# Optimization experiments

Hardware: AMD Instinct MI355X
Metric: run time of the kernel (lower is better)

## Reference

```python
import jax, jax.numpy as jnp
import numpy as np

B, S, D, H, DH, FF = 4, 4096, 1024, 16, 64, 2048
EPS = 1e-6


def setup_inputs() -> dict:
    key = jax.random.key(0)
    ks = jax.random.split(key, 8)
    s = 0.02
    return {
        "x": jax.random.normal(ks[0], (B, S, D), jnp.float32),
        "scale": jnp.ones((D,), jnp.float32),
        "qw": jax.random.normal(ks[1], (DH * H, D), jnp.float32) * s,
        "qb": jnp.zeros((DH * H,), jnp.float32),
        "kw": jax.random.normal(ks[2], (DH * H, D), jnp.float32) * s,
        "kb": jnp.zeros((DH * H,), jnp.float32),
        "vw": jax.random.normal(ks[3], (DH * H, D), jnp.float32) * s,
        "vb": jnp.zeros((DH * H,), jnp.float32),
        "ow": jax.random.normal(ks[4], (D, DH * H), jnp.float32) * s,
        "ob": jnp.zeros((D,), jnp.float32),
        "f1w": jax.random.normal(ks[5], (FF, D), jnp.float32) * s,
        "f1b": jnp.zeros((FF,), jnp.float32),
        "f2w": jax.random.normal(ks[6], (D, FF), jnp.float32) * s,
        "f2b": jnp.zeros((D,), jnp.float32),
    }


def reference(x, scale, qw, qb, kw, kb, vw, vb, ow, ob, f1w, f1b, f2w, f2b):
    def rms(h):
        return h / jnp.sqrt(jnp.mean(h * h, axis=-1, keepdims=True) + EPS) * scale

    # --- attention (faithful to the module's unusual permutes) ---
    xn = rms(x)
    q = (xn @ qw.T + qb).reshape(B, S, DH, H).transpose(0, 3, 2, 1)  # [B,H,DH,S]
    k = (xn @ kw.T + kb).reshape(B, S, DH, H).transpose(0, 3, 1, 2)  # [B,H,S,DH]
    v = (xn @ vw.T + vb).reshape(B, S, DH, H).transpose(0, 3, 2, 1)  # [B,H,DH,S]
    # scores contract over the SEQUENCE axis -> [B,H,DH,DH]
    att = jax.nn.softmax(jnp.einsum('bhds,bhse->bhde', q, k) / jnp.sqrt(jnp.float32(DH)), axis=-1)
    a = jnp.einsum('bhde,bhes->bhds', att, v)  # [B,H,DH,S]
    # torch: permute(0,2,1,3).reshape(B,-1,DH*H); row-major split of (DH,H,S) -> (S, DH*H)
    a = a.transpose(0, 2, 1, 3).reshape(B, S, DH * H)
    x = a @ ow.T + ob + x

    # --- FFN with the repo's 'SwiGLU' = x*sigmoid(x) + x ---
    xn = rms(x)
    h = xn @ f1w.T + f1b
    h = h * jax.nn.sigmoid(h) + h
    x = h @ f2w.T + f2b + x
    return x
```

## Files before the change

### kernel.cpp

```cpp
#include <hip/hip_runtime.h>
#include <math.h>

typedef unsigned short u16;
typedef __attribute__((ext_vector_type(4))) unsigned short us4;
typedef __attribute__((ext_vector_type(8))) unsigned short us8;
typedef __attribute__((ext_vector_type(4))) float f4;
typedef __attribute__((ext_vector_type(8))) short bf16x8;
typedef __attribute__((ext_vector_type(4))) float f32x4;

#define S_LEN   4096
#define D_MODEL 1024
#define N_HEAD  16
#define D_HEAD  64
#define FF_DIM  2048
#define TOKENS  16384

__device__ __forceinline__ float bf2f(u16 u) {
  union { float f; unsigned u; } x; x.u = ((unsigned)u) << 16; return x.f;
}
__device__ __forceinline__ u16 f2bf(float f) {
  union { float f; unsigned u; } x; x.f = f;
  return (u16)((x.u + 0x7FFFu + ((x.u >> 16) & 1u)) >> 16);
}

__device__ __forceinline__ void gll16(const void* g, void* l) {
  __builtin_amdgcn_global_load_lds(
      (const __attribute__((address_space(1))) void*)g,
      (__attribute__((address_space(3))) void*)l, 16, 0, 0);
}

#define BAR() __builtin_amdgcn_s_barrier()

__global__ void __launch_bounds__(256)
cvt6_k(const float* __restrict__ qw, const float* __restrict__ kw,
       const float* __restrict__ vw, const float* __restrict__ ow,
       const float* __restrict__ f1w, const float* __restrict__ f2w,
       const float* __restrict__ scale,
       u16* __restrict__ wq, u16* __restrict__ wk, u16* __restrict__ wv,
       u16* __restrict__ wo, u16* __restrict__ w1, u16* __restrict__ w2)
{
  const int id = blockIdx.x;
  const float* src; u16* dst; int base; bool fold;
  if      (id < 1024) { src = qw;  dst = wq; base = 0;    fold = true;  }
  else if (id < 2048) { src = kw;  dst = wk; base = 1024; fold = true;  }
  else if (id < 3072) { src = vw;  dst = wv; base = 2048; fold = true;  }
  else if (id < 4096) { src = ow;  dst = wo; base = 3072; fold = false; }
  else if (id < 6144) { src = f1w; dst = w1; base = 4096; fold = true;  }
  else                { src = f2w; dst = w2; base = 6144; fold = false; }
  const size_t i = ((size_t)(id - base) * 256 + threadIdx.x) * 4;
  const f4 v = *(const f4*)(src + i);
  f4 sc = {1.f, 1.f, 1.f, 1.f};
  if (fold) sc = *(const f4*)(scale + (i & 1023));
  us4 o;
  o[0] = f2bf(v[0] * sc[0]); o[1] = f2bf(v[1] * sc[1]);
  o[2] = f2bf(v[2] * sc[2]); o[3] = f2bf(v[3] * sc[3]);
  *(us4*)(dst + i) = o;
}

__global__ void __launch_bounds__(256)
cvtx_k(const float* __restrict__ in, u16* __restrict__ xb,
       float* __restrict__ invr)
{
  const int row = blockIdx.x;
  const int tid = threadIdx.x;
  const f4 v = *(const f4*)(in + (size_t)row * D_MODEL + tid * 4);
  float ss = v[0]*v[0] + v[1]*v[1] + v[2]*v[2] + v[3]*v[3];
#pragma unroll
  for (int off = 32; off > 0; off >>= 1) ss += __shfl_down(ss, off, 64);
  __shared__ float red[4];
  const int wid = tid >> 6, lane = tid & 63;
  if (lane == 0) red[wid] = ss;
  __syncthreads();
  if (tid == 0) {
    const float tot = red[0] + red[1] + red[2] + red[3];
    invr[row] = rsqrtf(tot * (1.0f / 1024.0f) + 1e-6f);
  }
  us4 o;
  o[0] = f2bf(v[0]); o[1] = f2bf(v[1]); o[2] = f2bf(v[2]); o[3] = f2bf(v[3]);
  *(us4*)(xb + (size_t)row * D_MODEL + tid * 4) = o;
}

template<int EPI>
__global__ __launch_bounds__(512, 2)
void g8k(const u16* __restrict__ Ag, const u16* __restrict__ Wg,
         const float* __restrict__ bq, const float* __restrict__ bk,
         const float* __restrict__ bv, const float* __restrict__ res,
         void* __restrict__ C0, void* __restrict__ C1, void* __restrict__ C2,
         int N, int K)
{
  __shared__ __align__(16) u16 lds[65536];
  const int tid = threadIdx.x;
  const int w = tid >> 6, l = tid & 63;
  const int fr = l & 15, fq = l >> 4;
  const int wm = w >> 2, wn = w & 3;
  const int m0 = blockIdx.x << 8, n0 = blockIdx.y << 8;
  const int srow = w * 8 + (l >> 3);
  const int scol = ((l & 7) ^ (l >> 3)) << 3;
  const int NT = K >> 6;

  auto STAGE = [&](int isA, int hf, int bfs, int nt) {
    const u16* G = isA ? Ag : Wg;
    const int rb = (isA ? m0 : n0) + hf * 128 + srow;
    const int ks = (nt < NT ? nt << 6 : 0) + scol;
    u16* lb = lds + (isA ? 0 : 32768) + bfs * 16384 + hf * 8192 + w * 512;
    gll16(G + (size_t)rb * K + ks, lb);
    gll16(G + (size_t)(rb + 64) * K + ks, lb + 4096);
  };

  f32x4 acc[8][4] = {};
  bf16x8 afr[4][2], bfr[2][2];

  auto LDA = [&](int bf, int mh) {
#pragma unroll
    for (int i = 0; i < 4; ++i)
#pragma unroll
      for (int kk = 0; kk < 2; ++kk)
        afr[i][kk] = *(const bf16x8*)(lds + bf * 16384 + mh * 8192
                                      + (i * 32 + wm * 16 + fr) * 64
                                      + ((kk * 32 + fq * 8) ^ ((fr & 7) << 3)));
  };
  auto LDB = [&](int bf, int nh) {
#pragma unroll
    for (int jn = 0; jn < 2; ++jn)
#pragma unroll
      for (int kk = 0; kk < 2; ++kk)
        bfr[jn][kk] = *(const bf16x8*)(lds + 32768 + bf * 16384 + nh * 8192
                                       + (jn * 64 + wn * 16 + fr) * 64
                                       + ((kk * 32 + fq * 8) ^ ((fr & 7) << 3)));
  };
  auto MM = [&](int mhalf, int nhalf) {
    __builtin_amdgcn_s_setprio(1);
#pragma unroll
    for (int i = 0; i < 4; ++i)
#pragma unroll
      for (int jn = 0; jn < 2; ++jn)
#pragma unroll
        for (int kk = 0; kk < 2; ++kk)
          acc[mhalf * 4 + i][nhalf * 2 + jn] =
              __builtin_amdgcn_mfma_f32_16x16x32_bf16(afr[i][kk], bfr[jn][kk],
                                                      acc[mhalf * 4 + i][nhalf * 2 + jn], 0, 0, 0);
    __builtin_amdgcn_s_setprio(0);
  };

  STAGE(1, 0, 0, 0);
  STAGE(0, 0, 0, 0);
  STAGE(0, 1, 0, 0);
  STAGE(1, 1, 0, 0);
  STAGE(1, 0, 1, 1);
  STAGE(1, 1, 1, 1);
  asm volatile("s_waitcnt vmcnt(4)" ::: "memory");
  BAR();

  const int NIT = K >> 7;
  for (int it = 0; it < NIT; ++it) {
#pragma unroll
    for (int hf2 = 0; hf2 < 2; ++hf2) {
      const int n = 2 * it + hf2;
      const int bf = n & 1;
      LDA(bf, 0); LDB(bf, 0);
      STAGE(0, 0, bf ^ 1, n + 1);
      BAR();
      MM(0, 0);
      BAR();
      LDB(bf, 1);
      STAGE(0, 1, bf ^ 1, n + 1);
      BAR();
      MM(0, 1);
      BAR();
      LDA(bf, 1);
      STAGE(1, 0, bf, n + 2);
      BAR();
      MM(1, 1);
      BAR();
      LDB(bf, 0);
      STAGE(1, 1, bf, n + 2);
      BAR();
      MM(1, 0);
      asm volatile("s_waitcnt vmcnt(4)" ::: "memory");
      BAR();
    }
  }
  asm volatile("s_waitcnt vmcnt(0)" ::: "memory");
  __builtin_amdgcn_s_barrier();
  asm volatile("" ::: "memory");

  if constexpr (EPI == 2) {
    float* C = (float*)C0;
#pragma unroll
    for (int mi = 0; mi < 8; ++mi)
#pragma unroll
      for (int ni = 0; ni < 4; ++ni) {
        const int c = n0 + ni * 64 + wn * 16 + fr;
        const int r0 = m0 + mi * 32 + wm * 16 + fq * 4;
        const float bb = bq[c];
#pragma unroll
        for (int j = 0; j < 4; ++j)
          C[(size_t)(r0 + j) * N + c] = acc[mi][ni][j] + bb + res[(size_t)(r0 + j) * N + c];
      }
  } else if constexpr (EPI == 4) {
    float* C = (float*)C0;
    u16* OB = (u16*)C1;
    float* SQ = (float*)C2;
#pragma unroll
    for (int mi = 0; mi < 8; ++mi) {
      const int r0 = m0 + mi * 32 + wm * 16 + fq * 4;
      float part0 = 0.f, part1 = 0.f, part2 = 0.f, part3 = 0.f;
#pragma unroll
      for (int ni = 0; ni < 4; ++ni) {
        const int c = n0 + ni * 64 + wn * 16 + fr;
        const float bb = bq[c];
#pragma unroll
        for (int j = 0; j < 4; ++j) {
          const float v = acc[mi][ni][j] + bb + res[(size_t)(r0 + j) * N + c];
          C[(size_t)(r0 + j) * N + c] = v;
          OB[(size_t)(r0 + j) * N + c] = f2bf(v);
          if (j == 0) part0 += v * v;
          else if (j == 1) part1 += v * v;
          else if (j == 2) part2 += v * v;
          else part3 += v * v;
        }
      }
      float part[4] = {part0, part1, part2, part3};
#pragma unroll
      for (int j = 0; j < 4; ++j) {
        float p = part[j];
        p += __shfl_xor(p, 1, 64);
        p += __shfl_xor(p, 2, 64);
        p += __shfl_xor(p, 4, 64);
        p += __shfl_xor(p, 8, 64);
        if (fr == 0) atomicAdd(&SQ[r0 + j], p);
      }
    }
  } else if constexpr (EPI == 3) {
    u16* C = (u16*)C0;
    const float* SQ = res;
#pragma unroll
    for (int mi = 0; mi < 8; ++mi) {
      const int r0 = m0 + mi * 32 + wm * 16 + fq * 4;
      const f4 sq4 = *(const f4*)(SQ + r0);
      float iv[4];
#pragma unroll
      for (int j = 0; j < 4; ++j) iv[j] = rsqrtf(sq4[j] * (1.0f / 1024.0f) + 1e-6f);
#pragma unroll
      for (int ni = 0; ni < 4; ++ni) {
        const int c = n0 + ni * 64 + wn * 16 + fr;
        const float bb = bq[c];
#pragma unroll
        for (int j = 0; j < 4; ++j) {
          const float v = acc[mi][ni][j] * iv[j] + bb;
          const float sig = 1.0f / (1.0f + expf(-v));
          C[(size_t)(r0 + j) * N + c] = f2bf(v * sig + v);
        }
      }
    }
  } else {
    const int z = blockIdx.y >> 2;
    const float* bias = z == 0 ? bq : (z == 1 ? bk : bv);
    const float* IV = res;
    const int n0l = n0 & 1023;
    const int bb = m0 >> 12, s0l = m0 & (S_LEN - 1);
#pragma unroll
    for (int mi = 0; mi < 8; ++mi)
#pragma unroll
      for (int ni = 0; ni < 4; ++ni) {
        const int c = ni * 64 + wn * 16 + fr;
        const int r0 = mi * 32 + wm * 16 + fq * 4;
        const f4 iv4 = *(const f4*)(IV + m0 + r0);
        const float bv_ = bias[n0l + c];
        us4 pk;
#pragma unroll
        for (int j = 0; j < 4; ++j) pk[j] = f2bf(acc[mi][ni][j] * iv4[j] + bv_);
        const int byte = ((c << 9) + (r0 << 1)) ^ ((c & 7) << 4);
        *(us4*)((char*)lds + byte) = pk;
      }
    __syncthreads();
    if (z < 2) {
      u16* Cout = z == 0 ? (u16*)C0 : (u16*)C1;
      const int c = tid & 255, half = tid >> 8;
      const int o = n0l + c, d = o >> 4, h = o & 15;
      const int xr = (c & 7) << 4;
      u16* dst = Cout + ((size_t)((bb << 10) + (h << 6) + d)) * S_LEN + s0l + half * 128;
#pragma unroll
      for (int u = 0; u < 16; ++u) {
        const int byte = ((c << 9) + (half << 8) + (u << 4)) ^ xr;
        const us8 v = *(const us8*)((char*)lds + byte);
        *(us8*)(dst + u * 8) = v;
      }
    } else {
      u16* Cv = (u16*)C2;
      const int d0 = n0l >> 4;
#pragma unroll
      for (int q2 = 0; q2 < 8; ++q2) {
        const int idx = q2 * 512 + tid;
        const int h = idx >> 8, r = idx & 255;
        const int xr = (h & 7) << 4;
        us8 lo, hi;
#pragma unroll
        for (int dl = 0; dl < 8; ++dl) {
          lo[dl] = *(const u16*)((char*)lds + ((((h + dl * 16) << 9) + (r << 1)) ^ xr));
          hi[dl] = *(const u16*)((char*)lds + ((((h + (dl + 8) * 16) << 9) + (r << 1)) ^ xr));
        }
        u16* dst = Cv + ((size_t)(bb * 16 + h) * S_LEN + s0l + r) * 64 + d0;
        *(us8*)dst = lo;
        *(us8*)(dst + 8) = hi;
      }
    }
  }
}

__global__ void __launch_bounds__(256)
att_sm_k(const u16* __restrict__ qt, const u16* __restrict__ kt,
         u16* __restrict__ P)
{
  __shared__ float red[4][64][64];
  const int bh = blockIdx.x;
  const int tid = threadIdx.x, w = tid >> 6, l = tid & 63;
  const int fr = l & 15, fq = l >> 4;
  const u16* Qb = qt + (size_t)bh * D_HEAD * S_LEN;
  const u16* Kb = kt + (size_t)bh * D_HEAD * S_LEN;
  f32x4 acc[4][4] = {};
  const int sb = w * 1024 + fq * 8;
  for (int ks = 0; ks < 32; ++ks) {
    const int s0 = sb + ks * 32;
    bf16x8 a[4], b[4];
#pragma unroll
    for (int m = 0; m < 4; ++m)
      a[m] = *(const bf16x8*)(Qb + (size_t)(m*16 + fr) * S_LEN + s0);
#pragma unroll
    for (int n = 0; n < 4; ++n)
      b[n] = *(const bf16x8*)(Kb + (size_t)(n*16 + fr) * S_LEN + s0);
#pragma unroll
    for (int m = 0; m < 4; ++m)
#pragma unroll
      for (int n = 0; n < 4; ++n)
        acc[m][n] = __builtin_amdgcn_mfma_f32_16x16x32_bf16(a[m], b[n], acc[m][n], 0, 0, 0);
  }
#pragma unroll
  for (int m = 0; m < 4; ++m)
#pragma unroll
    for (int n = 0; n < 4; ++n)
      *(f32x4*)&red[w][n*16 + fr][m*16 + fq*4] = acc[m][n];
  __syncthreads();

  const int d = tid >> 2, sub = tid & 3;
  float p[16];
  float mx = -1e30f;
#pragma unroll
  for (int i = 0; i < 16; ++i) {
    const int e = sub * 16 + i;
    float v = red[0][e][d] + red[1][e][d] + red[2][e][d] + red[3][e][d];
    v *= 0.125f;
    p[i] = v; mx = fmaxf(mx, v);
  }
  mx = fmaxf(mx, __shfl_xor(mx, 1, 64));
  mx = fmaxf(mx, __shfl_xor(mx, 2, 64));
  float sm = 0.0f;
#pragma unroll
  for (int i = 0; i < 16; ++i) { p[i] = expf(p[i] - mx); sm += p[i]; }
  sm += __shfl_xor(sm, 1, 64);
  sm += __shfl_xor(sm, 2, 64);
  const float inv = 1.0f / sm;
  us8 o0, o1;
#pragma unroll
  for (int i = 0; i < 8; ++i) { o0[i] = f2bf(p[i] * inv); o1[i] = f2bf(p[i+8] * inv); }
  u16* dst = P + (size_t)bh * 4096 + d * 64 + sub * 16;
  *(us8*)dst = o0;
  *(us8*)(dst + 8) = o1;
}

__global__ void __launch_bounds__(256)
pv2_k(const u16* __restrict__ P, const u16* __restrict__ v2,
      u16* __restrict__ ar)
{
  const int bh = blockIdx.x, sc = blockIdx.y;
  const int b = bh >> 4, h = bh & 15;
  const int tid = threadIdx.x, w = tid >> 6, l = tid & 63;
  const int fr = l & 15, fq = l >> 4;
  const u16* Pb = P + (size_t)bh * 4096;
  const u16* Vb = v2 + (size_t)bh * D_HEAD * S_LEN;

  bf16x8 a[4][2];
#pragma unroll
  for (int m = 0; m < 4; ++m)
#pragma unroll
    for (int ks = 0; ks < 2; ++ks)
      a[m][ks] = *(const bf16x8*)(Pb + (m*16 + fr) * 64 + ks*32 + fq*8);

  const int sw = sc * 512 + w * 128;
  f32x4 acc[8][4] = {};
#pragma unroll
  for (int n = 0; n < 8; ++n) {
    const u16* vp = Vb + (size_t)(sw + n*16 + fr) * 64 + fq*8;
    const bf16x8 b0 = *(const bf16x8*)(vp);
    const bf16x8 b1 = *(const bf16x8*)(vp + 32);
#pragma unroll
    for (int m = 0; m < 4; ++m)
      acc[n][m] = __builtin_amdgcn_mfma_f32_16x16x32_bf16(a[m][0], b0, acc[n][m], 0, 0, 0);
#pragma unroll
    for (int m = 0; m < 4; ++m)
      acc[n][m] = __builtin_amdgcn_mfma_f32_16x16x32_bf16(a[m][1], b1, acc[n][m], 0, 0, 0);
  }

  const int shi = sc >> 1;
  const int col0 = (sc & 1) * 512 + w * 128;
#pragma unroll
  for (int m = 0; m < 4; ++m)
#pragma unroll
    for (int j = 0; j < 4; ++j) {
      const int d = m*16 + fq*4 + j;
      const size_t base = ((size_t)b * 4096 + (d << 6) + (h << 2) + shi) * 1024 + col0;
#pragma unroll
      for (int n = 0; n < 8; ++n)
        ar[base + n*16 + fr] = f2bf(acc[n][m][j]);
    }
}

extern "C" void kernel_launch(void* const* d_in, const int* in_sizes, int n_in,
                              void* d_out, int out_size, void* d_ws, size_t ws_size,
                              hipStream_t stream)
{
  const float* x     = (const float*)d_in[0];
  const float* scale = (const float*)d_in[1];
  const float* qw = (const float*)d_in[2];
  const float* qb = (const float*)d_in[3];
  const float* kw = (const float*)d_in[4];
  const float* kb = (const float*)d_in[5];
  const float* vw = (const float*)d_in[6];
  const float* vb = (const float*)d_in[7];
  const float* ow = (const float*)d_in[8];
  const float* ob = (const float*)d_in[9];
  const float* f1w = (const float*)d_in[10];
  const float* f1b = (const float*)d_in[11];
  const float* f2w = (const float*)d_in[12];
  const float* f2b = (const float*)d_in[13];
  float* out = (float*)d_out;

  const size_t TOKD = (size_t)TOKENS * D_MODEL;
  const size_t WSZ1 = (size_t)D_MODEL * D_MODEL;
  const size_t WSZ2 = (size_t)FF_DIM * D_MODEL;
  u16* xb = (u16*)d_ws;
  u16* qt = xb + TOKD;
  u16* kt = qt + TOKD;
  u16* v2 = kt + TOKD;
  u16* wq = v2 + TOKD;
  u16* wk = wq + WSZ1;
  u16* wv = wk + WSZ1;
  u16* wo = wv + WSZ1;
  u16* w1 = wo + WSZ1;
  u16* w2 = w1 + WSZ2;
  u16* Patt = w2 + WSZ2;
  float* invr1 = (float*)(Patt + (size_t)64 * 64 * 64);
  float* sumsq = invr1 + TOKENS;
  u16* hbuf = kt;
  u16* ar = qt;
  u16* outb = xb;

  dim3 blk(256);
  dim3 blk8(512);

  hipMemsetAsync(sumsq, 0, TOKENS * sizeof(float), stream);
  cvt6_k<<<8192, blk, 0, stream>>>(qw, kw, vw, ow, f1w, f2w, scale,
                                   wq, wk, wv, wo, w1, w2);
  cvtx_k<<<TOKENS, blk, 0, stream>>>(x, xb, invr1);
  g8k<0><<<dim3(TOKENS / 256, 12), blk8, 0, stream>>>(
      xb, wq, qb, kb, vb, invr1, qt, kt, v2, 3072, D_MODEL);
  att_sm_k<<<64, blk, 0, stream>>>(qt, kt, Patt);
  pv2_k<<<dim3(64, 8), blk, 0, stream>>>(Patt, v2, ar);
  g8k<4><<<dim3(TOKENS / 256, D_MODEL / 256), blk8, 0, stream>>>(
      ar, wo, ob, nullptr, nullptr, x, out, outb, sumsq, D_MODEL, D_MODEL);
  g8k<3><<<dim3(TOKENS / 256, FF_DIM / 256), blk8, 0, stream>>>(
      outb, w1, f1b, nullptr, nullptr, sumsq, hbuf, nullptr, nullptr, FF_DIM, D_MODEL);
  g8k<2><<<dim3(TOKENS / 256, D_MODEL / 256), blk8, 0, stream>>>(
      hbuf, w2, f2b, nullptr, nullptr, out, out, nullptr, nullptr, D_MODEL, FF_DIM);
}
```

Measured before the change: 445.5 us.

## Load GEMM B operand directly from global, stage only A in LDS

The 256x256 GEMM kernel stops staging the weight (B) tile through LDS. Each wave now reads its B fragments straight from global memory per K-step, and only A is double-buffered in LDS, which halves LDS to 64KB. The fine-grained four-phase schedule with partial vmcnt waits is replaced by a simple loop with a full waitcnt and barrier per tile, and the QKV epilogue transpose is split into two 128-column chunks to fit the smaller LDS. This aims to cut LDS footprint and traffic, possibly allowing more occupancy. In exchange it risks exposed global-load latency and lost load/compute overlap.

```diff
diff --git a/kernel.cpp b/kernel.cpp
--- a/kernel.cpp
+++ b/kernel.cpp
@@ -29,7 +29,11 @@
       (__attribute__((address_space(3))) void*)l, 16, 0, 0);
 }
 
-#define BAR() __builtin_amdgcn_s_barrier()
+#define TILE_SYNC() do {                                            \
+  asm volatile("s_waitcnt vmcnt(0) lgkmcnt(0)" ::: "memory");       \
+  __builtin_amdgcn_s_barrier();                                     \
+  asm volatile("" ::: "memory");                                    \
+} while (0)
 
 __global__ void __launch_bounds__(256)
 cvt6_k(const float* __restrict__ qw, const float* __restrict__ kw,
@@ -88,7 +92,7 @@
          void* __restrict__ C0, void* __restrict__ C1, void* __restrict__ C2,
          int N, int K)
 {
-  __shared__ __align__(16) u16 lds[65536];
+  __shared__ __align__(16) u16 lds[32768];
   const int tid = threadIdx.x;
   const int w = tid >> 6, l = tid & 63;
   const int fr = l & 15, fq = l >> 4;
@@ -98,91 +102,50 @@
   const int scol = ((l & 7) ^ (l >> 3)) << 3;
   const int NT = K >> 6;
 
-  auto STAGE = [&](int isA, int hf, int bfs, int nt) {
-    const u16* G = isA ? Ag : Wg;
-    const int rb = (isA ? m0 : n0) + hf * 128 + srow;
+  auto STAGE_A = [&](int bfs, int nt) {
     const int ks = (nt < NT ? nt << 6 : 0) + scol;
-    u16* lb = lds + (isA ? 0 : 32768) + bfs * 16384 + hf * 8192 + w * 512;
-    gll16(G + (size_t)rb * K + ks, lb);
-    gll16(G + (size_t)(rb + 64) * K + ks, lb + 4096);
+#pragma unroll
+    for (int j = 0; j < 4; ++j)
+      gll16(Ag + (size_t)(m0 + j * 64 + srow) * K + ks,
+            lds + bfs * 16384 + j * 4096 + w * 512);
   };
 
   f32x4 acc[8][4] = {};
-  bf16x8 afr[4][2], bfr[2][2];
-
-  auto LDA = [&](int bf, int mh) {
-#pragma unroll
-    for (int i = 0; i < 4; ++i)
+  const u16* Bp = Wg + (size_t)(n0 + wn * 16 + fr) * K + fq * 8;
+  const size_t niStride = (size_t)64 * K;
+
+  STAGE_A(0, 0);
+  TILE_SYNC();
+
+  for (int t = 0; t < NT; ++t) {
+    const int bf = t & 1;
+    STAGE_A(bf ^ 1, t + 1);
+    bf16x8 bfr[4][2];
+#pragma unroll
+    for (int ni = 0; ni < 4; ++ni)
 #pragma unroll
       for (int kk = 0; kk < 2; ++kk)
-        afr[i][kk] = *(const bf16x8*)(lds + bf * 16384 + mh * 8192
-                                      + (i * 32 + wm * 16 + fr) * 64
-                                      + ((kk * 32 + fq * 8) ^ ((fr & 7) << 3)));
-  };
-  auto LDB = [&](int bf, int nh) {
-#pragma unroll
-    for (int jn = 0; jn < 2; ++jn)
+        bfr[ni][kk] = *(const bf16x8*)(Bp + ni * niStride + t * 64 + kk * 32);
+    bf16x8 afr[8][2];
+#pragma unroll
+    for (int mi = 0; mi < 8; ++mi)
 #pragma unroll
       for (int kk = 0; kk < 2; ++kk)
-        bfr[jn][kk] = *(const bf16x8*)(lds + 32768 + bf * 16384 + nh * 8192
-                                       + (jn * 64 + wn * 16 + fr) * 64
+        afr[mi][kk] = *(const bf16x8*)(lds + bf * 16384
+                                       + (mi * 32 + wm * 16 + fr) * 64
                                        + ((kk * 32 + fq * 8) ^ ((fr & 7) << 3)));
-  };
-  auto MM = [&](int mhalf, int nhalf) {
     __builtin_amdgcn_s_setprio(1);
 #pragma unroll
-    for (int i = 0; i < 4; ++i)
-#pragma unroll
-      for (int jn = 0; jn < 2; ++jn)
+    for (int mi = 0; mi < 8; ++mi)
+#pragma unroll
+      for (int ni = 0; ni < 4; ++ni)
 #pragma unroll
         for (int kk = 0; kk < 2; ++kk)
-          acc[mhalf * 4 + i][nhalf * 2 + jn] =
-              __builtin_amdgcn_mfma_f32_16x16x32_bf16(afr[i][kk], bfr[jn][kk],
-                                                      acc[mhalf * 4 + i][nhalf * 2 + jn], 0, 0, 0);
+          acc[mi][ni] = __builtin_amdgcn_mfma_f32_16x16x32_bf16(
+              afr[mi][kk], bfr[ni][kk], acc[mi][ni], 0, 0, 0);
     __builtin_amdgcn_s_setprio(0);
-  };
-
-  STAGE(1, 0, 0, 0);
-  STAGE(0, 0, 0, 0);
-  STAGE(0, 1, 0, 0);
-  STAGE(1, 1, 0, 0);
-  STAGE(1, 0, 1, 1);
-  STAGE(1, 1, 1, 1);
-  asm volatile("s_waitcnt vmcnt(4)" ::: "memory");
-  BAR();
-
-  const int NIT = K >> 7;
-  for (int it = 0; it < NIT; ++it) {
-#pragma unroll
-    for (int hf2 = 0; hf2 < 2; ++hf2) {
-      const int n = 2 * it + hf2;
-      const int bf = n & 1;
-      LDA(bf, 0); LDB(bf, 0);
-      STAGE(0, 0, bf ^ 1, n + 1);
-      BAR();
-      MM(0, 0);
-      BAR();
-      LDB(bf, 1);
-      STAGE(0, 1, bf ^ 1, n + 1);
-      BAR();
-      MM(0, 1);
-      BAR();
-      LDA(bf, 1);
-      STAGE(1, 0, bf, n + 2);
-      BAR();
-      MM(1, 1);
-      BAR();
-      LDB(bf, 0);
-      STAGE(1, 1, bf, n + 2);
-      BAR();
-      MM(1, 0);
-      asm volatile("s_waitcnt vmcnt(4)" ::: "memory");
-      BAR();
-    }
-  }
-  asm volatile("s_waitcnt vmcnt(0)" ::: "memory");
-  __builtin_amdgcn_s_barrier();
-  asm volatile("" ::: "memory");
+    TILE_SYNC();
+  }
 
   if constexpr (EPI == 2) {
     float* C = (float*)C0;
@@ -260,49 +223,52 @@
     const int n0l = n0 & 1023;
     const int bb = m0 >> 12, s0l = m0 & (S_LEN - 1);
 #pragma unroll
-    for (int mi = 0; mi < 8; ++mi)
-#pragma unroll
-      for (int ni = 0; ni < 4; ++ni) {
-        const int c = ni * 64 + wn * 16 + fr;
-        const int r0 = mi * 32 + wm * 16 + fq * 4;
-        const f4 iv4 = *(const f4*)(IV + m0 + r0);
-        const float bv_ = bias[n0l + c];
-        us4 pk;
-#pragma unroll
-        for (int j = 0; j < 4; ++j) pk[j] = f2bf(acc[mi][ni][j] * iv4[j] + bv_);
-        const int byte = ((c << 9) + (r0 << 1)) ^ ((c & 7) << 4);
-        *(us4*)((char*)lds + byte) = pk;
-      }
-    __syncthreads();
-    if (z < 2) {
-      u16* Cout = z == 0 ? (u16*)C0 : (u16*)C1;
-      const int c = tid & 255, half = tid >> 8;
-      const int o = n0l + c, d = o >> 4, h = o & 15;
-      const int xr = (c & 7) << 4;
-      u16* dst = Cout + ((size_t)((bb << 10) + (h << 6) + d)) * S_LEN + s0l + half * 128;
-#pragma unroll
-      for (int u = 0; u < 16; ++u) {
-        const int byte = ((c << 9) + (half << 8) + (u << 4)) ^ xr;
-        const us8 v = *(const us8*)((char*)lds + byte);
-        *(us8*)(dst + u * 8) = v;
-      }
-    } else {
-      u16* Cv = (u16*)C2;
-      const int d0 = n0l >> 4;
-#pragma unroll
-      for (int q2 = 0; q2 < 8; ++q2) {
-        const int idx = q2 * 512 + tid;
-        const int h = idx >> 8, r = idx & 255;
-        const int xr = (h & 7) << 4;
-        us8 lo, hi;
-#pragma unroll
-        for (int dl = 0; dl < 8; ++dl) {
-          lo[dl] = *(const u16*)((char*)lds + ((((h + dl * 16) << 9) + (r << 1)) ^ xr));
-          hi[dl] = *(const u16*)((char*)lds + ((((h + (dl + 8) * 16) << 9) + (r << 1)) ^ xr));
+    for (int ch = 0; ch < 2; ++ch) {
+      __syncthreads();
+#pragma unroll
+      for (int mi = 0; mi < 8; ++mi)
+#pragma unroll
+        for (int ni = 0; ni < 4; ++ni) {
+          const int c = ni * 64 + wn * 16 + fr;
+          if ((c >> 7) != ch) continue;
+          const int cp = c & 127;
+          const int r0 = mi * 32 + wm * 16 + fq * 4;
+          const f4 iv4 = *(const f4*)(IV + m0 + r0);
+          const float bv_ = bias[n0l + c];
+          us4 pk;
+#pragma unroll
+          for (int j = 0; j < 4; ++j) pk[j] = f2bf(acc[mi][ni][j] * iv4[j] + bv_);
+          const int byte = ((cp << 9) + (r0 << 1)) ^ ((cp & 7) << 4);
+          *(us4*)((char*)lds + byte) = pk;
         }
-        u16* dst = Cv + ((size_t)(bb * 16 + h) * S_LEN + s0l + r) * 64 + d0;
-        *(us8*)dst = lo;
-        *(us8*)(dst + 8) = hi;
+      __syncthreads();
+      if (z < 2) {
+        u16* Cout = z == 0 ? (u16*)C0 : (u16*)C1;
+        const int cp = tid & 127, seg = tid >> 7;
+        const int o = n0l + ch * 128 + cp, d = o >> 4, h = o & 15;
+        const int xr = (cp & 7) << 4;
+        u16* dst = Cout + ((size_t)((bb << 10) + (h << 6) + d)) * S_LEN + s0l + seg * 64;
+#pragma unroll
+        for (int u = 0; u < 8; ++u) {
+          const int byte = ((cp << 9) + (seg << 7) + (u << 4)) ^ xr;
+          const us8 v = *(const us8*)((char*)lds + byte);
+          *(us8*)(dst + u * 8) = v;
+        }
+      } else {
+        u16* Cv = (u16*)C2;
+        const int d0 = (n0l >> 4) + ch * 8;
+#pragma unroll
+        for (int q2 = 0; q2 < 8; ++q2) {
+          const int idx = q2 * 512 + tid;
+          const int h = idx >> 8, r = idx & 255;
+          const int xr = (h & 7) << 4;
+          us8 o8;
+#pragma unroll
+          for (int dl = 0; dl < 8; ++dl)
+            o8[dl] = *(const u16*)((char*)lds + ((((h + dl * 16) << 9) + (r << 1)) ^ xr));
+          u16* dst = Cv + ((size_t)(bb * 16 + h) * S_LEN + s0l + r) * 64 + d0;
+          *(us8*)dst = o8;
+        }
       }
     }
   }
```

After: 623.3 us. 1.4x slower.
